# Kernel tuning notes

Hardware: AMD Instinct MI355X
Metric: run time of the kernel (lower is better)

## Reference

```python
import jax, jax.numpy as jnp
import numpy as np

EMB = 64       # embedding_size
ATT = 32       # att_embedding_size (per-head dim)
HEADS = 4      # head_num
OUT = ATT * HEADS


def setup_inputs() -> dict:
    key = jax.random.key(0)
    ks = jax.random.split(key, 9)
    B, F = 16384, 40
    x = jax.random.normal(ks[0], (B, F, EMB), dtype=jnp.float32)
    # nn.Linear params: weight [out, in], bias [out]
    s = 0.05
    Wq = jax.random.normal(ks[1], (OUT, EMB), dtype=jnp.float32) * s
    bq = jax.random.normal(ks[2], (OUT,), dtype=jnp.float32) * s
    Wk = jax.random.normal(ks[3], (OUT, EMB), dtype=jnp.float32) * s
    bk = jax.random.normal(ks[4], (OUT,), dtype=jnp.float32) * s
    Wv = jax.random.normal(ks[5], (OUT, EMB), dtype=jnp.float32) * s
    bv = jax.random.normal(ks[6], (OUT,), dtype=jnp.float32) * s
    Wr = jax.random.normal(ks[7], (OUT, EMB), dtype=jnp.float32) * s
    br = jax.random.normal(ks[8], (OUT,), dtype=jnp.float32) * s
    return {"x": x, "Wq": Wq, "bq": bq, "Wk": Wk, "bk": bk,
            "Wv": Wv, "bv": bv, "Wr": Wr, "br": br}


def reference(x, Wq, bq, Wk, bk, Wv, bv, Wr, br):
    B, F, E = x.shape
    H, D = HEADS, ATT
    # QKV projections; split along last dim + cat along batch == reshape to heads
    q = (jnp.einsum('bfe,oe->bfo', x, Wq) + bq).reshape(B, F, H, D)
    k = (jnp.einsum('bfe,oe->bfo', x, Wk) + bk).reshape(B, F, H, D)
    v = (jnp.einsum('bfe,oe->bfo', x, Wv) + bv).reshape(B, F, H, D)
    # scaled dot-product attention over fields; NOTE: original scales by
    # sqrt(embedding_size), not sqrt(att_embedding_size)
    scale = 1.0 / jnp.sqrt(jnp.float32(E))
    att = jnp.einsum('bfhd,bghd->bhfg', q, k) * scale  # [B,H,F,F]
    att = jax.nn.softmax(att, axis=-1)                 # dropout_p = 0.0
    out = jnp.einsum('bhfg,bghd->bfhd', att, v).reshape(B, F, H * D)
    res = jnp.einsum('bfe,oe->bfo', x, Wr) + br        # use_res=True
    return jax.nn.relu(out + res)
```

## Files before the change

### kernel.cpp

```cpp
#include <hip/hip_runtime.h>
#include <hip/hip_bf16.h>


#define F_DIM 40
#define E_DIM 64
#define O_DIM 128

typedef __bf16 bf16x8 __attribute__((ext_vector_type(8)));
typedef float  f32x4  __attribute__((ext_vector_type(4)));

#define QO 0
#define KO 5440
#define VO 10880
#define RO 20096
#define UO 25536
#define PSZ 2880
#define TOT 37632

static __device__ __forceinline__ unsigned short f2bf(float f) {
  unsigned u = __builtin_bit_cast(unsigned, f);
  u += 0x7FFFu + ((u >> 16) & 1u);
  return (unsigned short)(u >> 16);
}
static __device__ __forceinline__ float bf2f(unsigned short h) {
  unsigned u = ((unsigned)h) << 16;
  return __builtin_bit_cast(float, u);
}
static __device__ __forceinline__ unsigned pk2(float a, float b) {
  return (unsigned)f2bf(a) | ((unsigned)f2bf(b) << 16);
}
union LdsVec { uint2 u2[2]; bf16x8 v; };
static __device__ __forceinline__ bf16x8 lds_ld8(const unsigned short* p) {
  LdsVec t;
  t.u2[0] = *reinterpret_cast<const uint2*>(p);
  t.u2[1] = *reinterpret_cast<const uint2*>(p + 4);
  return t.v;
}
static __device__ __forceinline__ f32x4 mfma16(bf16x8 a, bf16x8 b, f32x4 c) {
  return __builtin_amdgcn_mfma_f32_16x16x32_bf16(a, b, c, 0, 0, 0);
}

#if __has_builtin(__builtin_amdgcn_exp2f)
#define EXP2F __builtin_amdgcn_exp2f
#else
#define EXP2F exp2f
#endif
#if __has_builtin(__builtin_amdgcn_rcpf)
#define RCPF __builtin_amdgcn_rcpf
#else
#define RCPF(x) (1.0f / (x))
#endif

__global__ void convert_weights(const float* __restrict__ Wq, const float* __restrict__ Wk,
                                const float* __restrict__ Wv, const float* __restrict__ Wr,
                                unsigned short* __restrict__ ws) {
  int i = blockIdx.x * 256 + threadIdx.x;
  const float* src = (i < 8192) ? Wq : (i < 16384) ? Wk : (i < 24576) ? Wv : Wr;
  ws[i] = f2bf(src[i & 8191]);
}

__global__ __launch_bounds__(256, 2) void interact_kernel(
    const float* __restrict__ x, const unsigned short* __restrict__ wbf,
    const float* __restrict__ bq, const float* __restrict__ bk,
    const float* __restrict__ bv, const float* __restrict__ br,
    float* __restrict__ out) {
  __shared__ __align__(16) unsigned short sm[TOT];
  const int t = threadIdx.x;
  const int w = t >> 6;
  const int l = t & 63;
  const int c = l & 15;
  const int q = l >> 4;
  const int b = blockIdx.x;

  const float* xp = x + (size_t)b * (F_DIM * E_DIM);
  for (int i = t; i < 640; i += 256) {
    float4 v4 = reinterpret_cast<const float4*>(xp)[i];
    int f = i >> 4, e4 = (i & 15) << 2;
    uint2 pk; pk.x = pk2(v4.x, v4.y); pk.y = pk2(v4.z, v4.w);
    *reinterpret_cast<uint2*>(sm + UO + f * 72 + e4) = pk;
  }
  {
    uint2 z; z.x = 0; z.y = 0;
    for (int i = t; i < 144; i += 256)
      reinterpret_cast<uint2*>(sm + UO + 40 * 72)[i] = z;
    for (int i = t; i < 512; i += 256) {
      int d = i >> 2, j = i & 3;
      *reinterpret_cast<uint2*>(sm + VO + d * 72 + 48 + 4 * j) = z;
    }
  }
  __syncthreads();

  const unsigned short* Wg = wbf + w * 8192;
  const float* bias = (w == 0) ? bq : (w == 1) ? bk : (w == 2) ? bv : br;
  f32x4 z4 = {0.f, 0.f, 0.f, 0.f};

  if (w != 2) {
    bf16x8 bx[3][2];
#pragma unroll
    for (int nt = 0; nt < 3; ++nt)
#pragma unroll
      for (int ks = 0; ks < 2; ++ks)
        bx[nt][ks] = lds_ld8(sm + UO + (c + 16 * nt) * 72 + 8 * q + 32 * ks);
    f32x4 acc[8][3];
#pragma unroll
    for (int mt = 0; mt < 8; ++mt)
#pragma unroll
      for (int nt = 0; nt < 3; ++nt) acc[mt][nt] = z4;
#pragma unroll
    for (int mt = 0; mt < 8; ++mt) {
      bf16x8 a0 = *reinterpret_cast<const bf16x8*>(Wg + (c + 16 * mt) * 64 + 8 * q);
      bf16x8 a1 = *reinterpret_cast<const bf16x8*>(Wg + (c + 16 * mt) * 64 + 8 * q + 32);
#pragma unroll
      for (int nt = 0; nt < 3; ++nt) {
        acc[mt][nt] = mfma16(a0, bx[nt][0], acc[mt][nt]);
        acc[mt][nt] = mfma16(a1, bx[nt][1], acc[mt][nt]);
      }
    }
    const int dstO = (w == 0) ? QO : (w == 1) ? KO : RO;
#pragma unroll
    for (int mt = 0; mt < 8; ++mt) {
      float4 bb = *reinterpret_cast<const float4*>(bias + 16 * mt + 4 * q);
#pragma unroll
      for (int nt = 0; nt < 3; ++nt) {
        int f = c + 16 * nt;
        if (f < 40) {
          uint2 pk;
          pk.x = pk2(acc[mt][nt][0] + bb.x, acc[mt][nt][1] + bb.y);
          pk.y = pk2(acc[mt][nt][2] + bb.z, acc[mt][nt][3] + bb.w);
          *reinterpret_cast<uint2*>(sm + dstO + f * 136 + 16 * mt + 4 * q) = pk;
        }
      }
    }
  } else {
    bf16x8 ax[3][2];
#pragma unroll
    for (int mt = 0; mt < 3; ++mt)
#pragma unroll
      for (int ks = 0; ks < 2; ++ks)
        ax[mt][ks] = lds_ld8(sm + UO + (c + 16 * mt) * 72 + 8 * q + 32 * ks);
    f32x4 acc[3][8];
#pragma unroll
    for (int mt = 0; mt < 3; ++mt)
#pragma unroll
      for (int nt = 0; nt < 8; ++nt) acc[mt][nt] = z4;
#pragma unroll
    for (int nt = 0; nt < 8; ++nt) {
      bf16x8 b0 = *reinterpret_cast<const bf16x8*>(Wg + (c + 16 * nt) * 64 + 8 * q);
      bf16x8 b1 = *reinterpret_cast<const bf16x8*>(Wg + (c + 16 * nt) * 64 + 8 * q + 32);
#pragma unroll
      for (int mt = 0; mt < 3; ++mt) {
        acc[mt][nt] = mfma16(ax[mt][0], b0, acc[mt][nt]);
        acc[mt][nt] = mfma16(ax[mt][1], b1, acc[mt][nt]);
      }
    }
#pragma unroll
    for (int nt = 0; nt < 8; ++nt) {
      float bb = bias[c + 16 * nt];
#pragma unroll
      for (int mt = 0; mt < 3; ++mt) {
        uint2 pk;
        pk.x = pk2(acc[mt][nt][0] + bb, acc[mt][nt][1] + bb);
        pk.y = pk2(acc[mt][nt][2] + bb, acc[mt][nt][3] + bb);
        *reinterpret_cast<uint2*>(sm + VO + (c + 16 * nt) * 72 + 16 * mt + 4 * q) = pk;
      }
    }
  }
  __syncthreads();

  unsigned short* pb = sm + UO + w * PSZ;
  {
    bf16x8 ka[3], qb[3];
#pragma unroll
    for (int gt = 0; gt < 3; ++gt)
      ka[gt] = lds_ld8(sm + KO + (c + 16 * gt) * 136 + 32 * w + 8 * q);
#pragma unroll
    for (int ft = 0; ft < 3; ++ft)
      qb[ft] = lds_ld8(sm + QO + (c + 16 * ft) * 136 + 32 * w + 8 * q);
    f32x4 s[3][3];
#pragma unroll
    for (int gt = 0; gt < 3; ++gt)
#pragma unroll
      for (int ft = 0; ft < 3; ++ft)
        s[gt][ft] = mfma16(ka[gt], qb[ft], z4);
    const float cexp = 0.125f * 1.44269504f;
#pragma unroll
    for (int ft = 0; ft < 3; ++ft) {
      int f = c + 16 * ft;
      float m = -1e30f;
#pragma unroll
      for (int gt = 0; gt < 2; ++gt)
#pragma unroll
        for (int r = 0; r < 4; ++r) m = fmaxf(m, s[gt][ft][r]);
      if (q < 2) {
#pragma unroll
        for (int r = 0; r < 4; ++r) m = fmaxf(m, s[2][ft][r]);
      }
      m = fmaxf(m, __shfl_xor(m, 16, 64));
      m = fmaxf(m, __shfl_xor(m, 32, 64));
      float p[3][4]; float sum = 0.f;
#pragma unroll
      for (int gt = 0; gt < 3; ++gt)
#pragma unroll
        for (int r = 0; r < 4; ++r) {
          float pe = EXP2F((s[gt][ft][r] - m) * cexp);
          if (gt == 2 && q >= 2) pe = 0.f;
          p[gt][r] = pe; sum += pe;
        }
      sum += __shfl_xor(sum, 16, 64);
      sum += __shfl_xor(sum, 32, 64);
      float inv = RCPF(sum);
      if (f < 40) {
#pragma unroll
        for (int gt = 0; gt < 3; ++gt) {
          uint2 pk;
          pk.x = pk2(p[gt][0] * inv, p[gt][1] * inv);
          pk.y = pk2(p[gt][2] * inv, p[gt][3] * inv);
          *reinterpret_cast<uint2*>(pb + f * 72 + 16 * gt + 4 * q) = pk;
        }
      }
    }
    uint2 zz; zz.x = 0; zz.y = 0;
    for (int i = l; i < 160; i += 64) {
      int r = i >> 2, j = i & 3;
      *reinterpret_cast<uint2*>(pb + r * 72 + 48 + 4 * j) = zz;
    }
  }

  f32x4 o[3][2];
  {
    bf16x8 pa[3][2], vb[2][2];
#pragma unroll
    for (int mt = 0; mt < 3; ++mt)
#pragma unroll
      for (int ks = 0; ks < 2; ++ks)
        pa[mt][ks] = lds_ld8(pb + (c + 16 * mt) * 72 + 8 * q + 32 * ks);
#pragma unroll
    for (int nt = 0; nt < 2; ++nt)
#pragma unroll
      for (int ks = 0; ks < 2; ++ks)
        vb[nt][ks] = lds_ld8(sm + VO + (32 * w + c + 16 * nt) * 72 + 8 * q + 32 * ks);
#pragma unroll
    for (int mt = 0; mt < 3; ++mt)
#pragma unroll
      for (int nt = 0; nt < 2; ++nt) {
        f32x4 a = z4;
        a = mfma16(pa[mt][0], vb[nt][0], a);
        a = mfma16(pa[mt][1], vb[nt][1], a);
        o[mt][nt] = a;
      }
  }

  {
    float* ob = out + (size_t)b * (F_DIM * O_DIM) + 32 * w;
#pragma unroll
    for (int mt = 0; mt < 3; ++mt) {
      int f0 = 16 * mt + 4 * q;
      if (f0 < 40) {
#pragma unroll
        for (int nt = 0; nt < 2; ++nt) {
          int col = c + 16 * nt;
#pragma unroll
          for (int r = 0; r < 4; ++r) {
            float rv = bf2f(sm[RO + (f0 + r) * 136 + 32 * w + col]);
            float val = o[mt][nt][r] + rv;
            ob[(size_t)(f0 + r) * O_DIM + col] = fmaxf(val, 0.f);
          }
        }
      }
    }
  }
}

extern "C" void kernel_launch(void* const* d_in, const int* in_sizes, int n_in,
                              void* d_out, int out_size, void* d_ws, size_t ws_size,
                              hipStream_t stream) {
  const float* x  = (const float*)d_in[0];
  const float* Wq = (const float*)d_in[1];
  const float* bq = (const float*)d_in[2];
  const float* Wk = (const float*)d_in[3];
  const float* bk = (const float*)d_in[4];
  const float* Wv = (const float*)d_in[5];
  const float* bv = (const float*)d_in[6];
  const float* Wr = (const float*)d_in[7];
  const float* br = (const float*)d_in[8];
  unsigned short* wbf = (unsigned short*)d_ws;
  float* out = (float*)d_out;
  convert_weights<<<128, 256, 0, stream>>>(Wq, Wk, Wv, Wr, wbf);
  interact_kernel<<<16384, 256, 0, stream>>>(x, wbf, bq, bk, bv, br, out);
}
```

Measured before the change: 678.9 us.

## Restructure per-head work so each wave owns its head end to end

```diff
diff --git a/kernel.cpp b/kernel.cpp
--- a/kernel.cpp
+++ b/kernel.cpp
@@ -3,19 +3,17 @@
 
 
 #define F_DIM 40
-#define E_DIM 64
 #define O_DIM 128
 
 typedef __bf16 bf16x8 __attribute__((ext_vector_type(8)));
 typedef float  f32x4  __attribute__((ext_vector_type(4)));
 
-#define QO 0
-#define KO 5440
-#define VO 10880
-#define RO 20096
-#define UO 25536
-#define PSZ 2880
-#define TOT 37632
+#define XBS 72
+#define QS  40
+#define VTS 72
+#define HB0 3456
+#define HSZ 5504
+#define TOT 25472
 
 static __device__ __forceinline__ unsigned short f2bf(float f) {
   unsigned u = __builtin_bit_cast(unsigned, f);
@@ -29,12 +27,12 @@
 static __device__ __forceinline__ unsigned pk2(float a, float b) {
   return (unsigned)f2bf(a) | ((unsigned)f2bf(b) << 16);
 }
-union LdsVec { uint2 u2[2]; bf16x8 v; };
+union V8 { uint2 u2[2]; uint4 u4; unsigned u[4]; bf16x8 v; };
 static __device__ __forceinline__ bf16x8 lds_ld8(const unsigned short* p) {
-  LdsVec t;
-  t.u2[0] = *reinterpret_cast<const uint2*>(p);
-  t.u2[1] = *reinterpret_cast<const uint2*>(p + 4);
-  return t.v;
+  V8 t; t.u2[0] = *(const uint2*)p; t.u2[1] = *(const uint2*)(p + 4); return t.v;
+}
+static __device__ __forceinline__ bf16x8 lds_ld16(const unsigned short* p) {
+  V8 t; t.u4 = *(const uint4*)p; return t.v;
 }
 static __device__ __forceinline__ f32x4 mfma16(bf16x8 a, bf16x8 b, f32x4 c) {
   return __builtin_amdgcn_mfma_f32_16x16x32_bf16(a, b, c, 0, 0, 0);
@@ -59,7 +57,7 @@
   ws[i] = f2bf(src[i & 8191]);
 }
 
-__global__ __launch_bounds__(256, 2) void interact_kernel(
+__global__ __launch_bounds__(256, 3) void interact_kernel(
     const float* __restrict__ x, const unsigned short* __restrict__ wbf,
     const float* __restrict__ bq, const float* __restrict__ bk,
     const float* __restrict__ bv, const float* __restrict__ br,
@@ -71,203 +69,200 @@
   const int c = l & 15;
   const int q = l >> 4;
   const int b = blockIdx.x;
-
-  const float* xp = x + (size_t)b * (F_DIM * E_DIM);
+  f32x4 z4 = {0.f, 0.f, 0.f, 0.f};
+
+  const float* xp = x + (size_t)b * (F_DIM * 64);
   for (int i = t; i < 640; i += 256) {
     float4 v4 = reinterpret_cast<const float4*>(xp)[i];
     int f = i >> 4, e4 = (i & 15) << 2;
     uint2 pk; pk.x = pk2(v4.x, v4.y); pk.y = pk2(v4.z, v4.w);
-    *reinterpret_cast<uint2*>(sm + UO + f * 72 + e4) = pk;
+    *reinterpret_cast<uint2*>(sm + f * XBS + e4) = pk;
   }
   {
     uint2 z; z.x = 0; z.y = 0;
     for (int i = t; i < 144; i += 256)
-      reinterpret_cast<uint2*>(sm + UO + 40 * 72)[i] = z;
-    for (int i = t; i < 512; i += 256) {
-      int d = i >> 2, j = i & 3;
-      *reinterpret_cast<uint2*>(sm + VO + d * 72 + 48 + 4 * j) = z;
-    }
+      reinterpret_cast<uint2*>(sm + 40 * XBS)[i] = z;
   }
   __syncthreads();
 
-  const unsigned short* Wg = wbf + w * 8192;
-  const float* bias = (w == 0) ? bq : (w == 1) ? bk : (w == 2) ? bv : br;
-  f32x4 z4 = {0.f, 0.f, 0.f, 0.f};
-
-  if (w != 2) {
-    bf16x8 bx[3][2];
-#pragma unroll
-    for (int nt = 0; nt < 3; ++nt)
-#pragma unroll
-      for (int ks = 0; ks < 2; ++ks)
-        bx[nt][ks] = lds_ld8(sm + UO + (c + 16 * nt) * 72 + 8 * q + 32 * ks);
-    f32x4 acc[8][3];
-#pragma unroll
-    for (int mt = 0; mt < 8; ++mt)
-#pragma unroll
-      for (int nt = 0; nt < 3; ++nt) acc[mt][nt] = z4;
-#pragma unroll
-    for (int mt = 0; mt < 8; ++mt) {
-      bf16x8 a0 = *reinterpret_cast<const bf16x8*>(Wg + (c + 16 * mt) * 64 + 8 * q);
-      bf16x8 a1 = *reinterpret_cast<const bf16x8*>(Wg + (c + 16 * mt) * 64 + 8 * q + 32);
-#pragma unroll
-      for (int nt = 0; nt < 3; ++nt) {
-        acc[mt][nt] = mfma16(a0, bx[nt][0], acc[mt][nt]);
-        acc[mt][nt] = mfma16(a1, bx[nt][1], acc[mt][nt]);
-      }
-    }
-    const int dstO = (w == 0) ? QO : (w == 1) ? KO : RO;
-#pragma unroll
-    for (int mt = 0; mt < 8; ++mt) {
-      float4 bb = *reinterpret_cast<const float4*>(bias + 16 * mt + 4 * q);
-#pragma unroll
-      for (int nt = 0; nt < 3; ++nt) {
-        int f = c + 16 * nt;
-        if (f < 40) {
-          uint2 pk;
-          pk.x = pk2(acc[mt][nt][0] + bb.x, acc[mt][nt][1] + bb.y);
-          pk.y = pk2(acc[mt][nt][2] + bb.z, acc[mt][nt][3] + bb.w);
-          *reinterpret_cast<uint2*>(sm + dstO + f * 136 + 16 * mt + 4 * q) = pk;
-        }
-      }
-    }
-  } else {
-    bf16x8 ax[3][2];
-#pragma unroll
-    for (int mt = 0; mt < 3; ++mt)
-#pragma unroll
-      for (int ks = 0; ks < 2; ++ks)
-        ax[mt][ks] = lds_ld8(sm + UO + (c + 16 * mt) * 72 + 8 * q + 32 * ks);
-    f32x4 acc[3][8];
-#pragma unroll
-    for (int mt = 0; mt < 3; ++mt)
-#pragma unroll
-      for (int nt = 0; nt < 8; ++nt) acc[mt][nt] = z4;
-#pragma unroll
-    for (int nt = 0; nt < 8; ++nt) {
-      bf16x8 b0 = *reinterpret_cast<const bf16x8*>(Wg + (c + 16 * nt) * 64 + 8 * q);
-      bf16x8 b1 = *reinterpret_cast<const bf16x8*>(Wg + (c + 16 * nt) * 64 + 8 * q + 32);
-#pragma unroll
-      for (int mt = 0; mt < 3; ++mt) {
-        acc[mt][nt] = mfma16(ax[mt][0], b0, acc[mt][nt]);
-        acc[mt][nt] = mfma16(ax[mt][1], b1, acc[mt][nt]);
-      }
-    }
-#pragma unroll
-    for (int nt = 0; nt < 8; ++nt) {
-      float bb = bias[c + 16 * nt];
-#pragma unroll
-      for (int mt = 0; mt < 3; ++mt) {
-        uint2 pk;
-        pk.x = pk2(acc[mt][nt][0] + bb, acc[mt][nt][1] + bb);
-        pk.y = pk2(acc[mt][nt][2] + bb, acc[mt][nt][3] + bb);
-        *reinterpret_cast<uint2*>(sm + VO + (c + 16 * nt) * 72 + 16 * mt + 4 * q) = pk;
-      }
-    }
-  }
-  __syncthreads();
-
-  unsigned short* pb = sm + UO + w * PSZ;
-  {
-    bf16x8 ka[3], qb[3];
-#pragma unroll
-    for (int gt = 0; gt < 3; ++gt)
-      ka[gt] = lds_ld8(sm + KO + (c + 16 * gt) * 136 + 32 * w + 8 * q);
-#pragma unroll
-    for (int ft = 0; ft < 3; ++ft)
-      qb[ft] = lds_ld8(sm + QO + (c + 16 * ft) * 136 + 32 * w + 8 * q);
-    f32x4 s[3][3];
-#pragma unroll
-    for (int gt = 0; gt < 3; ++gt)
-#pragma unroll
-      for (int ft = 0; ft < 3; ++ft)
-        s[gt][ft] = mfma16(ka[gt], qb[ft], z4);
-    const float cexp = 0.125f * 1.44269504f;
-#pragma unroll
-    for (int ft = 0; ft < 3; ++ft) {
-      int f = c + 16 * ft;
-      float m = -1e30f;
-#pragma unroll
-      for (int gt = 0; gt < 2; ++gt)
-#pragma unroll
-        for (int r = 0; r < 4; ++r) m = fmaxf(m, s[gt][ft][r]);
-      if (q < 2) {
-#pragma unroll
-        for (int r = 0; r < 4; ++r) m = fmaxf(m, s[2][ft][r]);
-      }
-      m = fmaxf(m, __shfl_xor(m, 16, 64));
-      m = fmaxf(m, __shfl_xor(m, 32, 64));
-      float p[3][4]; float sum = 0.f;
-#pragma unroll
-      for (int gt = 0; gt < 3; ++gt)
-#pragma unroll
-        for (int r = 0; r < 4; ++r) {
-          float pe = EXP2F((s[gt][ft][r] - m) * cexp);
-          if (gt == 2 && q >= 2) pe = 0.f;
-          p[gt][r] = pe; sum += pe;
-        }
-      sum += __shfl_xor(sum, 16, 64);
-      sum += __shfl_xor(sum, 32, 64);
-      float inv = RCPF(sum);
-      if (f < 40) {
-#pragma unroll
-        for (int gt = 0; gt < 3; ++gt) {
-          uint2 pk;
-          pk.x = pk2(p[gt][0] * inv, p[gt][1] * inv);
-          pk.y = pk2(p[gt][2] * inv, p[gt][3] * inv);
-          *reinterpret_cast<uint2*>(pb + f * 72 + 16 * gt + 4 * q) = pk;
-        }
-      }
-    }
-    uint2 zz; zz.x = 0; zz.y = 0;
-    for (int i = l; i < 160; i += 64) {
-      int r = i >> 2, j = i & 3;
-      *reinterpret_cast<uint2*>(pb + r * 72 + 48 + 4 * j) = zz;
-    }
-  }
-
-  f32x4 o[3][2];
-  {
-    bf16x8 pa[3][2], vb[2][2];
-#pragma unroll
-    for (int mt = 0; mt < 3; ++mt)
-#pragma unroll
-      for (int ks = 0; ks < 2; ++ks)
-        pa[mt][ks] = lds_ld8(pb + (c + 16 * mt) * 72 + 8 * q + 32 * ks);
-#pragma unroll
-    for (int nt = 0; nt < 2; ++nt)
-#pragma unroll
-      for (int ks = 0; ks < 2; ++ks)
-        vb[nt][ks] = lds_ld8(sm + VO + (32 * w + c + 16 * nt) * 72 + 8 * q + 32 * ks);
-#pragma unroll
-    for (int mt = 0; mt < 3; ++mt)
-#pragma unroll
-      for (int nt = 0; nt < 2; ++nt) {
-        f32x4 a = z4;
-        a = mfma16(pa[mt][0], vb[nt][0], a);
-        a = mfma16(pa[mt][1], vb[nt][1], a);
-        o[mt][nt] = a;
-      }
-  }
-
-  {
-    float* ob = out + (size_t)b * (F_DIM * O_DIM) + 32 * w;
-#pragma unroll
-    for (int mt = 0; mt < 3; ++mt) {
-      int f0 = 16 * mt + 4 * q;
-      if (f0 < 40) {
-#pragma unroll
-        for (int nt = 0; nt < 2; ++nt) {
-          int col = c + 16 * nt;
-#pragma unroll
-          for (int r = 0; r < 4; ++r) {
-            float rv = bf2f(sm[RO + (f0 + r) * 136 + 32 * w + col]);
-            float val = o[mt][nt][r] + rv;
-            ob[(size_t)(f0 + r) * O_DIM + col] = fmaxf(val, 0.f);
+  const int hb = HB0 + w * HSZ;
+  unsigned short* Qb  = sm + hb;
+  unsigned short* Kb  = Qb + 1600;
+  unsigned short* Vtb = Qb + 3200;
+
+  bf16x8 xf[3][2];
+#pragma unroll
+  for (int nt = 0; nt < 3; ++nt)
+#pragma unroll
+    for (int ks = 0; ks < 2; ++ks)
+      xf[nt][ks] = lds_ld8(sm + (c + 16 * nt) * XBS + 32 * ks + 8 * q);
+
+  {
+    const unsigned short* Wm[2] = { wbf + 32 * w * 64, wbf + 8192 + 32 * w * 64 };
+    const float* Bp[2] = { bq, bk };
+    unsigned short* Db[2] = { Qb, Kb };
+#pragma unroll
+    for (int pr = 0; pr < 2; ++pr) {
+#pragma unroll
+      for (int mt = 0; mt < 2; ++mt) {
+        const unsigned short* wr0 = Wm[pr] + (16 * mt + c) * 64 + 8 * q;
+        bf16x8 a0 = *reinterpret_cast<const bf16x8*>(wr0);
+        bf16x8 a1 = *reinterpret_cast<const bf16x8*>(wr0 + 32);
+        float4 bb = *reinterpret_cast<const float4*>(Bp[pr] + 32 * w + 16 * mt + 4 * q);
+#pragma unroll
+        for (int nt = 0; nt < 3; ++nt) {
+          f32x4 acc = mfma16(a1, xf[nt][1], mfma16(a0, xf[nt][0], z4));
+          int f = c + 16 * nt;
+          if (f < 40) {
+            uint2 pk;
+            pk.x = pk2(acc[0] + bb.x, acc[1] + bb.y);
+            pk.y = pk2(acc[2] + bb.z, acc[3] + bb.w);
+            *reinterpret_cast<uint2*>(Db[pr] + f * QS + 16 * mt + 4 * q) = pk;
           }
         }
       }
     }
+  }
+#pragma unroll
+  for (int nt = 0; nt < 2; ++nt) {
+    const unsigned short* wr0 = wbf + 2 * 8192 + (32 * w + 16 * nt + c) * 64 + 8 * q;
+    bf16x8 b0 = *reinterpret_cast<const bf16x8*>(wr0);
+    bf16x8 b1 = *reinterpret_cast<const bf16x8*>(wr0 + 32);
+    float bb = bv[32 * w + c + 16 * nt];
+#pragma unroll
+    for (int mt = 0; mt < 3; ++mt) {
+      f32x4 acc = mfma16(xf[mt][1], b1, mfma16(xf[mt][0], b0, z4));
+      uint2 pk;
+      pk.x = pk2(acc[0] + bb, acc[1] + bb);
+      pk.y = pk2(acc[2] + bb, acc[3] + bb);
+      *reinterpret_cast<uint2*>(Vtb + (c + 16 * nt) * VTS + 16 * mt + 4 * q) = pk;
+    }
+  }
+  {
+    uint2 zz; zz.x = 0; zz.y = 0;
+#pragma unroll
+    for (int k2 = 0; k2 < 2; ++k2) {
+      int idx = l + 64 * k2, row = idx >> 2, g4 = idx & 3;
+      *reinterpret_cast<uint2*>(Vtb + row * VTS + 48 + 4 * g4) = zz;
+    }
+  }
+  unsigned rp[3][2][2];
+#pragma unroll
+  for (int nt = 0; nt < 2; ++nt) {
+    const unsigned short* wr0 = wbf + 3 * 8192 + (32 * w + 16 * nt + c) * 64 + 8 * q;
+    bf16x8 b0 = *reinterpret_cast<const bf16x8*>(wr0);
+    bf16x8 b1 = *reinterpret_cast<const bf16x8*>(wr0 + 32);
+#pragma unroll
+    for (int mt = 0; mt < 3; ++mt) {
+      f32x4 acc = mfma16(xf[mt][1], b1, mfma16(xf[mt][0], b0, z4));
+      rp[mt][nt][0] = pk2(acc[0], acc[1]);
+      rp[mt][nt][1] = pk2(acc[2], acc[3]);
+    }
+  }
+
+  f32x4 s[3][3];
+  {
+    bf16x8 kf[3], qf[3];
+#pragma unroll
+    for (int gt = 0; gt < 3; ++gt) kf[gt] = lds_ld16(Kb + (c + 16 * gt) * QS + 8 * q);
+#pragma unroll
+    for (int ft = 0; ft < 3; ++ft) qf[ft] = lds_ld16(Qb + (c + 16 * ft) * QS + 8 * q);
+#pragma unroll
+    for (int gt = 0; gt < 3; ++gt)
+#pragma unroll
+      for (int ft = 0; ft < 3; ++ft)
+        s[gt][ft] = mfma16(kf[gt], qf[ft], z4);
+  }
+  unsigned pp[3][3][2];
+  const float cexp = 0.125f * 1.44269504f;
+#pragma unroll
+  for (int ft = 0; ft < 3; ++ft) {
+    float m = -1e30f;
+#pragma unroll
+    for (int gt = 0; gt < 2; ++gt)
+#pragma unroll
+      for (int r = 0; r < 4; ++r) m = fmaxf(m, s[gt][ft][r]);
+    if (q < 2) {
+#pragma unroll
+      for (int r = 0; r < 4; ++r) m = fmaxf(m, s[2][ft][r]);
+    }
+    m = fmaxf(m, __shfl_xor(m, 16, 64));
+    m = fmaxf(m, __shfl_xor(m, 32, 64));
+    float p[3][4]; float sum = 0.f;
+#pragma unroll
+    for (int gt = 0; gt < 3; ++gt)
+#pragma unroll
+      for (int r = 0; r < 4; ++r) {
+        float pe = EXP2F((s[gt][ft][r] - m) * cexp);
+        if (gt == 2 && q >= 2) pe = 0.f;
+        p[gt][r] = pe; sum += pe;
+      }
+    sum += __shfl_xor(sum, 16, 64);
+    sum += __shfl_xor(sum, 32, 64);
+    float inv = RCPF(sum);
+#pragma unroll
+    for (int gt = 0; gt < 3; ++gt) {
+      pp[ft][gt][0] = pk2(p[gt][0] * inv, p[gt][1] * inv);
+      pp[ft][gt][1] = pk2(p[gt][2] * inv, p[gt][3] * inv);
+    }
+  }
+
+  bf16x8 pf[3][2];
+#pragma unroll
+  for (int mt = 0; mt < 3; ++mt) {
+    V8 f0, f1;
+#pragma unroll
+    for (int a = 0; a < 4; ++a) {
+      int src = 16 * ((2 * q + (a >> 1)) & 3) + c;
+      unsigned v0 = (unsigned)__shfl((int)pp[mt][0][a & 1], src, 64);
+      unsigned v1 = (unsigned)__shfl((int)pp[mt][1][a & 1], src, 64);
+      unsigned v2 = (unsigned)__shfl((int)pp[mt][2][a & 1], src, 64);
+      f0.u[a] = (q < 2) ? v0 : v1;
+      f1.u[a] = (q < 2) ? v2 : 0u;
+    }
+    pf[mt][0] = f0.v; pf[mt][1] = f1.v;
+  }
+
+  f32x4 o[3][2];
+  {
+    bf16x8 vb[2][2];
+#pragma unroll
+    for (int nt = 0; nt < 2; ++nt)
+#pragma unroll
+      for (int ks = 0; ks < 2; ++ks)
+        vb[nt][ks] = lds_ld16(Vtb + (c + 16 * nt) * VTS + 32 * ks + 8 * q);
+#pragma unroll
+    for (int mt = 0; mt < 3; ++mt)
+#pragma unroll
+      for (int nt = 0; nt < 2; ++nt)
+        o[mt][nt] = mfma16(pf[mt][1], vb[nt][1], mfma16(pf[mt][0], vb[nt][0], z4));
+  }
+
+  float* os = reinterpret_cast<float*>(sm + hb);
+  float brv0 = br[32 * w + c], brv1 = br[32 * w + c + 16];
+#pragma unroll
+  for (int mt = 0; mt < 3; ++mt) {
+    if (mt < 2 || q < 2) {
+#pragma unroll
+      for (int nt = 0; nt < 2; ++nt) {
+        float bb = nt ? brv1 : brv0;
+#pragma unroll
+        for (int r = 0; r < 4; ++r) {
+          int f = 16 * mt + 4 * q + r;
+          unsigned pr_ = rp[mt][nt][r >> 1];
+          float rv = bf2f((unsigned short)((r & 1) ? (pr_ >> 16) : (pr_ & 0xFFFFu)));
+          os[f * QS + c + 16 * nt] = fmaxf(o[mt][nt][r] + rv + bb, 0.f);
+        }
+      }
+    }
+  }
+  float* op = out + (size_t)b * (F_DIM * O_DIM) + 32 * w;
+#pragma unroll
+  for (int it = 0; it < 5; ++it) {
+    int i = 64 * it + l;
+    int f = i >> 3, d4 = i & 7;
+    float4 v = *reinterpret_cast<const float4*>(os + f * QS + 4 * d4);
+    *reinterpret_cast<float4*>(op + (size_t)f * O_DIM + 4 * d4) = v;
   }
 }
 
```

Result: faster. 597.9 us (-11.9%).
